# Performance work log

Measured on AMD Instinct MI355X. Metric: run time of the kernel, lower is better.

Reference implementation:

```python
import jax, jax.numpy as jnp
import numpy as np

D = 256      # n_feature
LVL = 17     # tree depth (leaf levels)
MIX = 20     # M mixture components


def _lstm_cell(x, h, c, Wih, Whh, bih, bhh):
    # torch.nn.LSTMCell gate order: i, f, g, o
    g = x @ Wih.T + bih + h @ Whh.T + bhh
    i, f, gg, o = jnp.split(g, 4, axis=1)
    c2 = jax.nn.sigmoid(f) * c + jax.nn.sigmoid(i) * jnp.tanh(gg)
    return jax.nn.sigmoid(o) * jnp.tanh(c2), c2


def _get_parameter(y, M):
    parts = jnp.split(y[:, :13 * M], 13, axis=1)
    pi = jax.nn.softmax(parts[0], axis=1)
    mu_x, mu_y = parts[1], parts[2]
    sx, sy = jnp.exp(parts[3]), jnp.exp(parts[4])
    rho_xy = jnp.tanh(parts[5])
    mu_a, mu_b = parts[6], parts[7]
    sa, sb = jnp.exp(parts[8]), jnp.exp(parts[9])
    rho_ab = jnp.tanh(parts[10])
    mu_s, ss = parts[11], jnp.exp(parts[12])
    q = jax.nn.softmax(y[:, -3:], axis=1)
    return (pi, mu_x, mu_y, sx, sy, rho_xy, mu_a, mu_b, sa, sb, rho_ab, mu_s, ss, q)


def _bvn_logpdf(dx, dy, mx, my, sx, sy, rho):
    zx = (dx - mx) / sx
    zy = (dy - my) / sy
    Z = zx ** 2 + zy ** 2 - 2.0 * rho * zx * zy
    return -Z / (2.0 * (1.0 - rho ** 2)) - jnp.log(2.0 * jnp.pi * sx * sy * jnp.sqrt(1.0 - rho ** 2))


def _nll(pt, prm):
    # pt: [n, 8] = (x, y, a, b, slope, p1, p2, p3); prm: GMM parameters, each [n, M]
    pi, mx, my, sx, sy, rxy, ma, mb, sa, sb, rab, ms, ss, q = prm
    lpi = jnp.log(pi)
    dx, dy, da, db, ds = (pt[:, k:k + 1] for k in range(5))
    p = pt[:, 5:8]
    lse = jax.scipy.special.logsumexp
    lxy = lse(lpi + _bvn_logpdf(dx, dy, mx, my, sx, sy, rxy), axis=1)
    lab = lse(lpi + _bvn_logpdf(da, db, ma, mb, sa, sb, rab), axis=1)
    lsl = lse(lpi - (ds - ms) ** 2 / (2.0 * ss ** 2) - jnp.log(jnp.sqrt(2.0 * jnp.pi) * ss), axis=1)
    pen = -(p * jnp.log(q)).sum(axis=1)
    return -(lxy + lab + lsl) + pen


def _expected_pos(prm):
    pi, mx, my, sx, sy, rxy, ma, mb, sa, sb, rab, ms, ss, q = prm
    e = lambda m: (pi * m).sum(axis=1)
    return jnp.concatenate([jnp.stack([e(mx), e(my), e(ma), e(mb), e(ms)], axis=1), q], axis=1)


def _levels(I_flat):
    # I_flat is bottom-up concatenation of per-level [ni,3] blocks of a full binary tree
    n_int = I_flat.shape[0]
    L = int(np.log2(n_int + 1))
    sizes = [2 ** (L - 1 - i) for i in range(L)]
    offs = np.concatenate([[0], np.cumsum(sizes)])
    return [I_flat[offs[i]:offs[i + 1]] for i in range(L)]


def setup_inputs() -> dict:
    key = jax.random.key(0)
    ks = jax.random.split(key, 16)
    N = 2 ** (LVL + 1) - 1  # 262143 total nodes
    # heap-layout full binary tree: children of i are 2i+1, 2i+2; bottom-up levels
    blocks = []
    for l in range(LVL - 1, -1, -1):
        f = np.arange(2 ** l - 1, 2 ** (l + 1) - 1)
        blocks.append(np.stack([2 * f + 1, 2 * f + 2, f], axis=1))
    I_flat = jnp.asarray(np.concatenate(blocks, 0), dtype=jnp.int32)
    s = 0.05
    return {
        "X": jax.random.normal(ks[0], (N, 8), jnp.float32),
        "Feature": jax.random.normal(ks[1], (N, D), jnp.float32),
        "I_flat": I_flat,
        "W_ih_e": jax.random.normal(ks[2], (4 * (D // 2), 8), jnp.float32) * s,
        "W_hh_e": jax.random.normal(ks[3], (4 * (D // 2), D // 2), jnp.float32) * s,
        "b_ih_e": jax.random.normal(ks[4], (4 * (D // 2),), jnp.float32) * s,
        "b_hh_e": jax.random.normal(ks[5], (4 * (D // 2),), jnp.float32) * s,
        "fc_h_W": jax.random.normal(ks[6], (2 * D, D), jnp.float32) * s,
        "fc_h_b": jax.random.normal(ks[7], (2 * D,), jnp.float32) * s,
        "W_ih_d": jax.random.normal(ks[8], (4 * D, D + 8), jnp.float32) * s,
        "W_hh_d": jax.random.normal(ks[9], (4 * D, D), jnp.float32) * s,
        "b_ih_d": jax.random.normal(ks[10], (4 * D,), jnp.float32) * s,
        "b_hh_d": jax.random.normal(ks[11], (4 * D,), jnp.float32) * s,
        "fc_W": jax.random.normal(ks[12], (13 * MIX + 3, D // 2), jnp.float32) * s,
        "fc_b": jax.random.normal(ks[13], (13 * MIX + 3,), jnp.float32) * s,
    }


def reference(X, Feature, I_flat, W_ih_e, W_hh_e, b_ih_e, b_hh_e,
              fc_h_W, fc_h_b, W_ih_d, W_hh_d, b_ih_d, b_hh_d, fc_W, fc_b):
    levels = _levels(I_flat)
    num_I = len(levels)

    # ---- encode: bottom-up gather children -> LSTMCell -> scatter father ----
    Feature_New = Feature
    for I in levels:
        li, ri, fi = I[:, 0], I[:, 1], I[:, 2]
        hl, cl = jnp.split(Feature[li], 2, axis=1)
        hr, cr = jnp.split(Feature[ri], 2, axis=1)
        hlo, clo = _lstm_cell(X[li], hl, cl, W_ih_e, W_hh_e, b_ih_e, b_hh_e)
        hro, cro = _lstm_cell(X[ri], hr, cr, W_ih_e, W_hh_e, b_ih_e, b_hh_e)
        out = jnp.concatenate([hlo + hro, clo + cro], axis=1)
        Feature_New = Feature_New.at[fi].set(out)

    # ---- decode: top-down gather father -> LSTMCell+GMM head -> scatter children ----
    X_P = X
    Feat = Feature_New
    Loss = jnp.float32(0.0)
    for I in reversed(levels):
        li, ri, fi = I[:, 0], I[:, 1], I[:, 2]
        p_l, p_r, p_f = X[li], X[ri], X[fi]
        f_f = Feat[fi]
        z = jnp.tanh(f_f @ fc_h_W.T + fc_h_b)
        h_f, c_f = jnp.split(z, 2, axis=1)
        h_o, c_o = _lstm_cell(jnp.concatenate([p_f, f_f], axis=1), h_f, c_f,
                              W_ih_d, W_hh_d, b_ih_d, b_hh_d)
        h_left, h_right = jnp.split(h_o, 2, axis=1)
        c_left, c_right = jnp.split(c_o, 2, axis=1)
        prm_l = _get_parameter(h_left @ fc_W.T + fc_b, MIX)
        prm_r = _get_parameter(h_right @ fc_W.T + fc_b, MIX)
        direct = _nll(p_l, prm_l) + _nll(p_r, prm_r)
        swapped = _nll(p_l, prm_r) + _nll(p_r, prm_l)
        sw = swapped < direct  # l_r_index == 1 -> swap left/right outputs
        Loss = Loss + jnp.mean(jnp.where(sw, swapped, direct))
        pos_l, pos_r = _expected_pos(prm_l), _expected_pos(prm_r)
        feat_l = jnp.concatenate([h_left, c_left], axis=1)
        feat_r = jnp.concatenate([h_right, c_right], axis=1)
        swc = sw[:, None]
        Feat = Feat.at[li].set(jnp.where(swc, feat_r, feat_l))
        Feat = Feat.at[ri].set(jnp.where(swc, feat_l, feat_r))
        X_P = X_P.at[li].set(jnp.where(swc, pos_r, pos_l))
        X_P = X_P.at[ri].set(jnp.where(swc, pos_l, pos_r))
    return Loss / num_I
```

## Files before the change

kernel.cpp:

```cpp
#include <hip/hip_runtime.h>
#include <hip/hip_bf16.h>
#include <math.h>


#define LOG2PI 1.8378770664093453f

typedef __attribute__((ext_vector_type(8))) short short8;
typedef __attribute__((ext_vector_type(4))) float f32x4;

__device__ inline float frcp(float x) { return __builtin_amdgcn_rcpf(x); }
__device__ inline float fexp(float x) { return __expf(x); }
__device__ inline float flog(float x) { return __logf(x); }
__device__ inline float ftanh(float x) {
    float xc = fminf(fmaxf(x, -10.f), 10.f);
    float e = __expf(2.f * xc);
    return (e - 1.f) * frcp(e + 1.f);
}
__device__ inline float sigm(float x) {
    float xc = fminf(fmaxf(x, -30.f), 30.f);
    return frcp(1.f + __expf(-xc));
}

__device__ inline ushort f2b(float v) {
    union { float f; unsigned u; } x; x.f = v;
    unsigned r = x.u + 0x7fffu + ((x.u >> 16) & 1u);
    return (ushort)(r >> 16);
}
__device__ inline float b2f(ushort h) {
    union { unsigned u; float f; } x; x.u = ((unsigned)h) << 16; return x.f;
}

__device__ inline void gload16(const void* g, void* l) {
    __builtin_amdgcn_global_load_lds(
        (const __attribute__((address_space(1))) unsigned*)g,
        (__attribute__((address_space(3))) unsigned*)l, 16, 0, 0);
}

__device__ inline f32x4 mfma16(short8 a, short8 b, f32x4 c) {
    return __builtin_amdgcn_mfma_f32_16x16x32_bf16(a, b, c, 0, 0, 0);
}

__device__ inline float halfmax(float v) {
    #pragma unroll
    for (int o = 16; o >= 1; o >>= 1) v = fmaxf(v, __shfl_xor(v, o));
    return v;
}
__device__ inline float halfsum(float v) {
    #pragma unroll
    for (int o = 16; o >= 1; o >>= 1) v += __shfl_xor(v, o);
    return v;
}
__device__ inline float lse20(float t) {
    float m = halfmax(t);
    float s = halfsum(fexp(t - m));
    return m + flog(s);
}

__device__ inline float nll_node(const float* yb, const float* X,
                                 long long fi, int lane, bool& sw_out)
{
    const int half = lane >> 5, k = lane & 31;
    float v = (k < 20) ? yb[k] : -INFINITY;
    float mm = halfmax(v);
    float se = halfsum((k < 20) ? fexp(v - mm) : 0.f);
    float lpi = v - mm - flog(se);
    float mx = 0, my = 0, rsx = 1, rsy = 1, rho = 0, hro = 0, cxy = 0;
    float ma = 0, mb2 = 0, rsa = 1, rsb = 1, rab = 0, hra = 0, cab = 0;
    float ms = 0, hrs = 0, csl = 0;
    if (k < 20) {
        mx = yb[20 + k]; my = yb[40 + k];
        float lsx = yb[60 + k], lsy = yb[80 + k];
        rsx = fexp(-lsx); rsy = fexp(-lsy);
        rho = ftanh(yb[100 + k]);
        float omr = 1.f - rho * rho;
        hro = 0.5f * frcp(omr);
        cxy = LOG2PI + lsx + lsy + 0.5f * flog(omr);
        ma = yb[120 + k]; mb2 = yb[140 + k];
        float lsa = yb[160 + k], lsb = yb[180 + k];
        rsa = fexp(-lsa); rsb = fexp(-lsb);
        rab = ftanh(yb[200 + k]);
        float omr2 = 1.f - rab * rab;
        hra = 0.5f * frcp(omr2);
        cab = LOG2PI + lsa + lsb + 0.5f * flog(omr2);
        ms = yb[220 + k]; float lss = yb[240 + k];
        float rss = fexp(-lss);
        hrs = 0.5f * rss * rss;
        csl = 0.5f * LOG2PI + lss;
    }
    float lq0, lq1, lq2;
    {
        float q0 = yb[260], q1 = yb[261], q2 = yb[262];
        float qm = fmaxf(q0, fmaxf(q1, q2));
        float l = flog(fexp(q0 - qm) + fexp(q1 - qm) + fexp(q2 - qm)) + qm;
        lq0 = q0 - l; lq1 = q1 - l; lq2 = q2 - l;
    }
    const float* pl = X + (size_t)(2 * fi + 1) * 8;
    const float* pr = X + (size_t)(2 * fi + 2) * 8;
    float res[2];
    #pragma unroll
    for (int s = 0; s < 2; ++s) {
        const float* pt = s ? pr : pl;
        float dx = pt[0], dy = pt[1], da = pt[2], db = pt[3], ds = pt[4];
        float t1 = -INFINITY, t2 = -INFINITY, t3 = -INFINITY;
        if (k < 20) {
            float zx = (dx - mx) * rsx, zy = (dy - my) * rsy;
            float Zz = zx * zx + zy * zy - 2.f * rho * zx * zy;
            t1 = lpi - Zz * hro - cxy;
            float za = (da - ma) * rsa, zb = (db - mb2) * rsb;
            float Z2 = za * za + zb * zb - 2.f * rab * za * zb;
            t2 = lpi - Z2 * hra - cab;
            float zs = ds - ms;
            t3 = lpi - zs * zs * hrs - csl;
        }
        float l1 = lse20(t1), l2 = lse20(t2), l3 = lse20(t3);
        float pen = -(pt[5] * lq0 + pt[6] * lq1 + pt[7] * lq2);
        res[s] = -(l1 + l2 + l3) + pen;
    }
    float Aval = half ? res[1] : res[0];
    float Bval = half ? res[0] : res[1];
    float direct = Aval + __shfl_xor(Aval, 32);
    float swapped = Bval + __shfl_xor(Bval, 32);
    sw_out = swapped < direct;
    return sw_out ? swapped : direct;
}

__device__ inline void feat_write_ap(ushort* Ap, const ushort* Hj,
                                     const ushort* Cj, long long fi, bool sw,
                                     int lane)
{
    const size_t rowL = 2 * (size_t)fi + 1;
    const int offL = sw ? 128 : 0;
    const int offR = 128 - offL;
    const int part = lane >> 5;
    const int c = (lane & 31) * 4;
    ushort4 vL = *(const ushort4*)((part ? Cj : Hj) + offL + c);
    ushort4 vR = *(const ushort4*)((part ? Cj : Hj) + offR + c);
    *(ushort4*)(Ap + rowL * 576 + 8 + part * 128 + c) = vL;
    *(ushort4*)(Ap + (rowL + 1) * 576 + 8 + part * 128 + c) = vR;
}

__global__ __launch_bounds__(256) void z_gemm(
    ushort* __restrict__ Apc,
    const ushort* __restrict__ Wz,
    const float* __restrict__ fc_h_b,
    ushort* __restrict__ Zcc,
    int M)
{
    __shared__ ushort As[128 * 64];
    __shared__ ushort Bs[128 * 64];
    const int tid = threadIdx.x;
    const int lane = tid & 63;
    const int w = tid >> 6;
    const int wr = w >> 1, wc = w & 1;
    const int fr = lane & 15, fq = lane >> 4;
    const int m0 = blockIdx.x * 128, n0 = blockIdx.y * 128;

    f32x4 acc[4][4] = {};

    #pragma unroll
    for (int k0 = 0; k0 < 256; k0 += 64) {
        __syncthreads();
        #pragma unroll
        for (int it = 0; it < 4; ++it) {
            const int i = it * 256 + tid;
            const int row = i >> 3, slot = i & 7;
            const int sl = slot ^ (row & 7);
            const int wbase = (i - lane) * 8;
            {
                int gm = m0 + row; gm = gm < M ? gm : M - 1;
                gload16(Apc + (size_t)gm * 576 + 8 + k0 + sl * 8, &As[wbase]);
            }
            {
                int gn = n0 + row; gn = gn < 512 ? gn : 511;
                gload16(Wz + (size_t)gn * 256 + k0 + sl * 8, &Bs[wbase]);
            }
        }
        __syncthreads();
        #pragma unroll
        for (int ks = 0; ks < 2; ++ks) {
            short8 af[4], bfr[4];
            #pragma unroll
            for (int mr = 0; mr < 4; ++mr) {
                const int row = wr * 64 + mr * 16 + fr;
                const int sl = (ks * 4 + fq) ^ (row & 7);
                af[mr] = *(const short8*)&As[row * 64 + sl * 8];
            }
            #pragma unroll
            for (int nc = 0; nc < 4; ++nc) {
                const int row = wc * 64 + nc * 16 + fr;
                const int sl = (ks * 4 + fq) ^ (row & 7);
                bfr[nc] = *(const short8*)&Bs[row * 64 + sl * 8];
            }
            #pragma unroll
            for (int mr = 0; mr < 4; ++mr)
                #pragma unroll
                for (int nc = 0; nc < 4; ++nc)
                    acc[mr][nc] = mfma16(af[mr], bfr[nc], acc[mr][nc]);
        }
    }

    #pragma unroll
    for (int mr = 0; mr < 4; ++mr) {
        #pragma unroll
        for (int j = 0; j < 4; ++j) {
            const int row = m0 + wr * 64 + mr * 16 + fq * 4 + j;
            if (row >= M) continue;
            #pragma unroll
            for (int nc = 0; nc < 4; ++nc) {
                const int col = n0 + wc * 64 + nc * 16 + fr;
                const float z = ftanh(acc[mr][nc][j] + fc_h_b[col]);
                if (col < 256)
                    Apc[(size_t)row * 576 + 264 + col] = f2b(z);
                else
                    Zcc[(size_t)row * 256 + (col - 256)] = f2b(z);
            }
        }
    }
}

__global__ __launch_bounds__(256) void gates_lstm(
    const ushort* __restrict__ Apc,
    const ushort* __restrict__ Wg,
    const float*  __restrict__ bg,
    const ushort* __restrict__ Zcc,
    ushort* __restrict__ H, ushort* __restrict__ C, int M)
{
    __shared__ ushort As[128 * 64];
    __shared__ ushort Bs[128 * 64];
    const int tid = threadIdx.x;
    const int lane = tid & 63;
    const int w = tid >> 6;
    const int wr = w >> 1, wc = w & 1;
    const int fr = lane & 15, fq = lane >> 4;
    const int m0 = blockIdx.x * 128, n0 = blockIdx.y * 128;

    f32x4 acc[4][4] = {};

    #pragma unroll
    for (int k0 = 0; k0 < 576; k0 += 64) {
        __syncthreads();
        #pragma unroll
        for (int it = 0; it < 4; ++it) {
            const int i = it * 256 + tid;
            const int row = i >> 3, slot = i & 7;
            const int sl = slot ^ (row & 7);
            const int wbase = (i - lane) * 8;
            {
                int gm = m0 + row; gm = gm < M ? gm : M - 1;
                gload16(Apc + (size_t)gm * 576 + k0 + sl * 8, &As[wbase]);
            }
            gload16(Wg + (size_t)(n0 + row) * 576 + k0 + sl * 8, &Bs[wbase]);
        }
        __syncthreads();
        #pragma unroll
        for (int ks = 0; ks < 2; ++ks) {
            short8 af[4], bfr[4];
            #pragma unroll
            for (int mr = 0; mr < 4; ++mr) {
                const int row = wr * 64 + mr * 16 + fr;
                const int sl = (ks * 4 + fq) ^ (row & 7);
                af[mr] = *(const short8*)&As[row * 64 + sl * 8];
            }
            #pragma unroll
            for (int nc = 0; nc < 4; ++nc) {
                const int row = wc * 64 + nc * 16 + fr;
                const int sl = (ks * 4 + fq) ^ (row & 7);
                bfr[nc] = *(const short8*)&Bs[row * 64 + sl * 8];
            }
            #pragma unroll
            for (int mr = 0; mr < 4; ++mr)
                #pragma unroll
                for (int nc = 0; nc < 4; ++nc)
                    acc[mr][nc] = mfma16(af[mr], bfr[nc], acc[mr][nc]);
        }
    }

    const int q = fr & 3;
    #pragma unroll
    for (int mr = 0; mr < 4; ++mr) {
        const int node = m0 + wr * 64 + mr * 16 + fq * 4 + q;
        #pragma unroll
        for (int nc = 0; nc < 4; ++nc) {
            const int col = n0 + wc * 64 + nc * 16 + fr;
            f32x4 v = acc[mr][nc];
            const float b = bg[col];
            v[0] += b; v[1] += b; v[2] += b; v[3] += b;
            float gv[4];
            gv[q] = v[q];
            #pragma unroll
            for (int m = 1; m < 4; ++m)
                gv[q ^ m] = __shfl_xor(v[q ^ m], m);
            if (node < M) {
                const int t = (col >> 2) & 255;
                const float cf = b2f(Zcc[(size_t)node * 256 + t]);
                const float c2 = sigm(gv[1]) * cf + sigm(gv[0]) * ftanh(gv[2]);
                const float hv = sigm(gv[3]) * ftanh(c2);
                H[(size_t)node * 256 + t] = f2b(hv);
                C[(size_t)node * 256 + t] = f2b(c2);
            }
        }
    }
}

__global__ __launch_bounds__(256) void ynll(
    const ushort* __restrict__ Hb, const ushort* __restrict__ Cc,
    const ushort* __restrict__ Wyp,
    const float* __restrict__ fc_b, const float* __restrict__ X,
    ushort* __restrict__ Ap, float* __restrict__ loss,
    int Bc, long long nb_fi, float scale, int writeFeat)
{
    __shared__ ushort Hs[32 * 128];
    __shared__ float Ys[32][324];
    __shared__ float lsum[4];
    const int tid = threadIdx.x;
    const int lane = tid & 63;
    const int wv = tid >> 6;
    const int fr = lane & 15, fq = lane >> 4;
    const int n16 = blockIdx.x * 16;

    #pragma unroll
    for (int it = 0; it < 2; ++it) {
        const int i = it * 256 + tid;
        const int row = i >> 4, slot = i & 15;
        const int sl = slot ^ (row & 7);
        int gr = n16 * 2 + row;
        const int grmax = 2 * Bc - 1;
        gr = gr <= grmax ? gr : grmax;
        gload16(Hb + (size_t)gr * 128 + sl * 8, &Hs[(i - lane) * 8]);
    }
    __syncthreads();

    f32x4 acc[2][5] = {};
    #pragma unroll
    for (int ks = 0; ks < 4; ++ks) {
        short8 a[2];
        #pragma unroll
        for (int rf = 0; rf < 2; ++rf) {
            const int row = rf * 16 + fr;
            const int sl = (ks * 4 + fq) ^ (row & 7);
            a[rf] = *(const short8*)&Hs[row * 128 + sl * 8];
        }
        #pragma unroll
        for (int n = 0; n < 5; ++n) {
            const short8 b = *(const short8*)(
                Wyp + (size_t)(wv * 80 + n * 16 + fr) * 128 + ks * 32 + fq * 8);
            acc[0][n] = mfma16(a[0], b, acc[0][n]);
            acc[1][n] = mfma16(a[1], b, acc[1][n]);
        }
    }
    #pragma unroll
    for (int rf = 0; rf < 2; ++rf)
        #pragma unroll
        for (int n = 0; n < 5; ++n)
            #pragma unroll
            for (int j = 0; j < 4; ++j) {
                const int row = rf * 16 + fq * 4 + j;
                const int col = wv * 80 + n * 16 + fr;
                Ys[row][col] = acc[rf][n][j] + (col < 263 ? fc_b[col] : 0.f);
            }
    __syncthreads();

    float wsum = 0.f;
    #pragma unroll
    for (int s4 = 0; s4 < 4; ++s4) {
        const int jj = wv * 4 + s4;
        const int j = n16 + jj;
        if (j >= Bc) break;
        bool sw;
        const long long fi = nb_fi + j;
        wsum += nll_node(Ys[2 * jj + (lane >> 5)], X, fi, lane, sw);
        if (writeFeat)
            feat_write_ap(Ap, Hb + (size_t)j * 256, Cc + (size_t)j * 256,
                          fi, sw, lane);
    }
    if (lane == 0) lsum[wv] = wsum;
    __syncthreads();
    if (tid == 0)
        atomicAdd(loss, (lsum[0] + lsum[1] + lsum[2] + lsum[3]) * scale);
}

__global__ __launch_bounds__(256) void pack_all(
    const float* __restrict__ fc_h_W, ushort* __restrict__ Wz,
    const float* __restrict__ Wih, const float* __restrict__ Whh,
    ushort* __restrict__ Wg,
    const float* __restrict__ bih, const float* __restrict__ bhh,
    float* __restrict__ bg,
    const float* __restrict__ fcW, ushort* __restrict__ Wy,
    const float* __restrict__ X, ushort* __restrict__ Ap, int nInt)
{
    int i = blockIdx.x * 256 + threadIdx.x;
    if (i < 131072) { Wz[i] = f2b(fc_h_W[i]); return; }
    i -= 131072;
    if (i < 589824) {
        int np = i / 576, c = i - np * 576;
        int n = (np & 3) * 256 + (np >> 2);
        float v = 0.f;
        if (c < 264) v = Wih[n * 264 + c];
        else if (c < 520) v = Whh[n * 256 + (c - 264)];
        Wg[i] = f2b(v);
        return;
    }
    i -= 589824;
    if (i < 1024) {
        int n = (i & 3) * 256 + (i >> 2);
        bg[i] = bih[n] + bhh[n];
        return;
    }
    i -= 1024;
    if (i < 40960) {
        int r = i / 128;
        Wy[i] = f2b(r < 263 ? fcW[i] : 0.f);
        return;
    }
    i -= 40960;
    if (i < nInt * 64) {
        int row = i >> 6, c = i & 63;
        if (c < 8) Ap[(size_t)row * 576 + c] = f2b(X[row * 8 + c]);
        else       Ap[(size_t)row * 576 + 512 + c] = 0;
    }
}

__global__ __launch_bounds__(256) void encoder_root(
    const float* __restrict__ X, const float* __restrict__ Feature,
    const float* __restrict__ Wih, const float* __restrict__ Whh,
    const float* __restrict__ bih, const float* __restrict__ bhh,
    ushort* __restrict__ Ap)
{
    __shared__ float gsh[2][512];
    __shared__ float hc[2][256];
    const int t = threadIdx.x;
    for (int ch = 0; ch < 2; ++ch) {
        const int node = 1 + ch;
        const float* x = X + node * 8;
        const float* h = Feature + (size_t)node * 256;
        #pragma unroll
        for (int gi = 0; gi < 2; ++gi) {
            int g = t + gi * 256;
            float s = bih[g] + bhh[g];
            const float* wi = Wih + (size_t)g * 8;
            #pragma unroll
            for (int k = 0; k < 8; ++k) s += wi[k] * x[k];
            const float* wh = Whh + (size_t)g * 128;
            for (int k = 0; k < 128; ++k) s += wh[k] * h[k];
            gsh[ch][g] = s;
        }
    }
    __syncthreads();
    {
        int ch = t >> 7, u = t & 127;
        float i_ = gsh[ch][u], f_ = gsh[ch][128 + u];
        float gg = gsh[ch][256 + u], o_ = gsh[ch][384 + u];
        float c = Feature[(size_t)(1 + ch) * 256 + 128 + u];
        float c2 = sigm(f_) * c + sigm(i_) * ftanh(gg);
        hc[ch][u] = sigm(o_) * ftanh(c2);
        hc[ch][128 + u] = c2;
    }
    __syncthreads();
    Ap[8 + t] = f2b(hc[0][t] + hc[1][t]);
}

extern "C" void kernel_launch(void* const* d_in, const int* in_sizes, int n_in,
                              void* d_out, int out_size, void* d_ws, size_t ws_size,
                              hipStream_t stream)
{
    const float* X       = (const float*)d_in[0];
    const float* Feature = (const float*)d_in[1];
    const float* W_ih_e  = (const float*)d_in[3];
    const float* W_hh_e  = (const float*)d_in[4];
    const float* b_ih_e  = (const float*)d_in[5];
    const float* b_hh_e  = (const float*)d_in[6];
    const float* fc_h_W  = (const float*)d_in[7];
    const float* fc_h_b  = (const float*)d_in[8];
    const float* W_ih_d  = (const float*)d_in[9];
    const float* W_hh_d  = (const float*)d_in[10];
    const float* b_ih_d  = (const float*)d_in[11];
    const float* b_hh_d  = (const float*)d_in[12];
    const float* fc_W    = (const float*)d_in[13];
    const float* fc_b    = (const float*)d_in[14];
    const int Nnodes = in_sizes[0] / 8;
    const int nInt = (Nnodes - 1) / 2;

    float* out = (float*)d_out;
    hipMemsetAsync(d_out, 0, sizeof(float), stream);

    char* cur = (char*)d_ws;
    auto take = [&](size_t bytes) {
        char* p = cur;
        cur += (bytes + 255) & ~(size_t)255;
        return p;
    };
    ushort* Ap = (ushort*)take((size_t)(nInt + 1) * 576 * 2);
    ushort* Wz = (ushort*)take((size_t)512 * 256 * 2);
    ushort* Wg = (ushort*)take((size_t)1024 * 576 * 2);
    ushort* Wy = (ushort*)take((size_t)320 * 128 * 2);
    float*  bg = (float*) take((size_t)1024 * 4);
    const size_t fixed_used = (size_t)(cur - (char*)d_ws);
    int CB = 65536;
    while (CB > 8192 && fixed_used + (size_t)CB * 1536 + 4096 > ws_size) CB >>= 1;
    ushort* Zcc = (ushort*)take((size_t)CB * 256 * 2);
    ushort* Hb  = (ushort*)take((size_t)CB * 256 * 2);
    ushort* Cc  = (ushort*)take((size_t)CB * 256 * 2);

    const int packTotal = 131072 + 589824 + 1024 + 40960 + nInt * 64;
    pack_all<<<(packTotal + 255) / 256, 256, 0, stream>>>(
        fc_h_W, Wz, W_ih_d, W_hh_d, Wg, b_ih_d, b_hh_d, bg, fc_W, Wy,
        X, Ap, nInt);

    encoder_root<<<1, 256, 0, stream>>>(X, Feature, W_ih_e, W_hh_e,
                                        b_ih_e, b_hh_e, Ap);

    for (int l = 0; l < 17; ++l) {
        const int B = 1 << l;
        const long long nb = B - 1;
        const int writeFeat = (l < 16) ? 1 : 0;
        const float scale = 1.f / ((float)B * 17.f);
        for (int j0 = 0; j0 < B; j0 += CB) {
            const int Bc = (B - j0 < CB) ? (B - j0) : CB;
            const int mg = (Bc + 127) / 128;
            ushort* Apc = Ap + (size_t)(nb + j0) * 576;
            z_gemm<<<dim3(mg, 4), 256, 0, stream>>>(Apc, Wz, fc_h_b, Zcc, Bc);
            gates_lstm<<<dim3(mg, 8), 256, 0, stream>>>(
                Apc, Wg, bg, Zcc, Hb, Cc, Bc);
            ynll<<<(Bc + 15) / 16, 256, 0, stream>>>(
                Hb, Cc, Wy, fc_b, X, Ap, out,
                Bc, nb + j0, scale, writeFeat);
        }
    }
}
```

Before: 1.316 ms.

## Fuse next-level z_gemm into ynll epilogue and drop chunked launches

The per-level z_gemm launch is removed. Each ynll block now computes the tanh(fc_h) projection for the child rows it just wrote, storing them into Ap and Zcc for the next level, with a single z_gemm launched for the root. The Y logits are kept in shared memory as bf16, so one aliased pool can hold H, Y and the feature tiles. Chunking by CB is dropped and Zcc/Hb/Cc are sized to a fixed 65536 rows, which assumes the workspace is large enough. The Ap padding init is also vectorised. This cuts one launch per level and an extra global round trip, but it adds serial GEMM work to the tail of ynll and lowers Y precision.

```diff
diff --git a/kernel.cpp b/kernel.cpp
--- a/kernel.cpp
+++ b/kernel.cpp
@@ -56,11 +56,11 @@
     return m + flog(s);
 }
 
-__device__ inline float nll_node(const float* yb, const float* X,
+__device__ inline float nll_node(const ushort* yb, const float* X,
                                  long long fi, int lane, bool& sw_out)
 {
     const int half = lane >> 5, k = lane & 31;
-    float v = (k < 20) ? yb[k] : -INFINITY;
+    float v = (k < 20) ? b2f(yb[k]) : -INFINITY;
     float mm = halfmax(v);
     float se = halfsum((k < 20) ? fexp(v - mm) : 0.f);
     float lpi = v - mm - flog(se);
@@ -68,28 +68,28 @@
     float ma = 0, mb2 = 0, rsa = 1, rsb = 1, rab = 0, hra = 0, cab = 0;
     float ms = 0, hrs = 0, csl = 0;
     if (k < 20) {
-        mx = yb[20 + k]; my = yb[40 + k];
-        float lsx = yb[60 + k], lsy = yb[80 + k];
+        mx = b2f(yb[20 + k]); my = b2f(yb[40 + k]);
+        float lsx = b2f(yb[60 + k]), lsy = b2f(yb[80 + k]);
         rsx = fexp(-lsx); rsy = fexp(-lsy);
-        rho = ftanh(yb[100 + k]);
+        rho = ftanh(b2f(yb[100 + k]));
         float omr = 1.f - rho * rho;
         hro = 0.5f * frcp(omr);
         cxy = LOG2PI + lsx + lsy + 0.5f * flog(omr);
-        ma = yb[120 + k]; mb2 = yb[140 + k];
-        float lsa = yb[160 + k], lsb = yb[180 + k];
+        ma = b2f(yb[120 + k]); mb2 = b2f(yb[140 + k]);
+        float lsa = b2f(yb[160 + k]), lsb = b2f(yb[180 + k]);
         rsa = fexp(-lsa); rsb = fexp(-lsb);
-        rab = ftanh(yb[200 + k]);
+        rab = ftanh(b2f(yb[200 + k]));
         float omr2 = 1.f - rab * rab;
         hra = 0.5f * frcp(omr2);
         cab = LOG2PI + lsa + lsb + 0.5f * flog(omr2);
-        ms = yb[220 + k]; float lss = yb[240 + k];
+        ms = b2f(yb[220 + k]); float lss = b2f(yb[240 + k]);
         float rss = fexp(-lss);
         hrs = 0.5f * rss * rss;
         csl = 0.5f * LOG2PI + lss;
     }
     float lq0, lq1, lq2;
     {
-        float q0 = yb[260], q1 = yb[261], q2 = yb[262];
+        float q0 = b2f(yb[260]), q1 = b2f(yb[261]), q2 = b2f(yb[262]);
         float qm = fmaxf(q0, fmaxf(q1, q2));
         float l = flog(fexp(q0 - qm) + fexp(q1 - qm) + fexp(q2 - qm)) + qm;
         lq0 = q0 - l; lq1 = q1 - l; lq2 = q2 - l;
@@ -302,16 +302,22 @@
     }
 }
 
-__global__ __launch_bounds__(256) void ynll(
+#define YS 272
+__global__ __launch_bounds__(256) void ynll_z(
     const ushort* __restrict__ Hb, const ushort* __restrict__ Cc,
     const ushort* __restrict__ Wyp,
     const float* __restrict__ fc_b, const float* __restrict__ X,
-    ushort* __restrict__ Ap, float* __restrict__ loss,
+    ushort* __restrict__ Ap,
+    const ushort* __restrict__ Wz, const float* __restrict__ fc_h_b,
+    ushort* __restrict__ Zcc,
+    float* __restrict__ loss,
     int Bc, long long nb_fi, float scale, int writeFeat)
 {
-    __shared__ ushort Hs[32 * 128];
-    __shared__ float Ys[32][324];
+    __shared__ char pool[17408] __attribute__((aligned(16)));
     __shared__ float lsum[4];
+    ushort* Hs  = (ushort*)pool;
+    ushort* Ysb = (ushort*)pool;
+    ushort* Fs  = (ushort*)pool;
     const int tid = threadIdx.x;
     const int lane = tid & 63;
     const int wv = tid >> 6;
@@ -348,6 +354,8 @@
             acc[1][n] = mfma16(a[1], b, acc[1][n]);
         }
     }
+    __syncthreads();
+
     #pragma unroll
     for (int rf = 0; rf < 2; ++rf)
         #pragma unroll
@@ -356,7 +364,8 @@
             for (int j = 0; j < 4; ++j) {
                 const int row = rf * 16 + fq * 4 + j;
                 const int col = wv * 80 + n * 16 + fr;
-                Ys[row][col] = acc[rf][n][j] + (col < 263 ? fc_b[col] : 0.f);
+                if (col < 263)
+                    Ysb[row * YS + col] = f2b(acc[rf][n][j] + fc_b[col]);
             }
     __syncthreads();
 
@@ -368,7 +377,7 @@
         if (j >= Bc) break;
         bool sw;
         const long long fi = nb_fi + j;
-        wsum += nll_node(Ys[2 * jj + (lane >> 5)], X, fi, lane, sw);
+        wsum += nll_node(&Ysb[(2 * jj + (lane >> 5)) * YS], X, fi, lane, sw);
         if (writeFeat)
             feat_write_ap(Ap, Hb + (size_t)j * 256, Cc + (size_t)j * 256,
                           fi, sw, lane);
@@ -377,6 +386,53 @@
     __syncthreads();
     if (tid == 0)
         atomicAdd(loss, (lsum[0] + lsum[1] + lsum[2] + lsum[3]) * scale);
+
+    if (!writeFeat) return;
+
+    const size_t base = 2 * (size_t)(nb_fi + n16) + 1;
+    const int rmax = 2 * Bc - 2 * n16 - 1;
+    #pragma unroll
+    for (int it = 0; it < 4; ++it) {
+        const int i = it * 256 + tid;
+        const int row = i >> 5, slot = i & 31;
+        const int sl = slot ^ (row & 7);
+        int r = row; r = r <= rmax ? r : rmax;
+        gload16(Ap + (base + r) * 576 + 8 + sl * 8, &Fs[(i - lane) * 8]);
+    }
+    __syncthreads();
+
+    f32x4 zacc[2][8] = {};
+    for (int ks = 0; ks < 8; ++ks) {
+        short8 a[2];
+        #pragma unroll
+        for (int mf = 0; mf < 2; ++mf) {
+            const int r = mf * 16 + fr;
+            const int ss = (ks * 4 + fq) ^ (r & 7);
+            a[mf] = *(const short8*)&Fs[r * 256 + ss * 8];
+        }
+        #pragma unroll
+        for (int nf = 0; nf < 8; ++nf) {
+            const short8 b = *(const short8*)(
+                Wz + (size_t)(wv * 128 + nf * 16 + fr) * 256 + ks * 32 + fq * 8);
+            zacc[0][nf] = mfma16(a[0], b, zacc[0][nf]);
+            zacc[1][nf] = mfma16(a[1], b, zacc[1][nf]);
+        }
+    }
+    #pragma unroll
+    for (int mf = 0; mf < 2; ++mf)
+        #pragma unroll
+        for (int nf = 0; nf < 8; ++nf)
+            #pragma unroll
+            for (int j = 0; j < 4; ++j) {
+                const int r = mf * 16 + fq * 4 + j;
+                if (r > rmax) continue;
+                const int col = wv * 128 + nf * 16 + fr;
+                const float z = ftanh(zacc[mf][nf][j] + fc_h_b[col]);
+                if (col < 256)
+                    Ap[(base + r) * 576 + 264 + col] = f2b(z);
+                else
+                    Zcc[(size_t)(2 * n16 + r) * 256 + (col - 256)] = f2b(z);
+            }
 }
 
 __global__ __launch_bounds__(256) void pack_all(
@@ -413,10 +469,19 @@
         return;
     }
     i -= 40960;
-    if (i < nInt * 64) {
-        int row = i >> 6, c = i & 63;
-        if (c < 8) Ap[(size_t)row * 576 + c] = f2b(X[row * 8 + c]);
-        else       Ap[(size_t)row * 576 + 512 + c] = 0;
+    if (i < nInt * 8) {
+        int row = i >> 3, s = i & 7;
+        if (s == 0) {
+            const float* xs = X + (size_t)row * 8;
+            short8 v;
+            #pragma unroll
+            for (int k = 0; k < 8; ++k)
+                ((ushort*)&v)[k] = f2b(xs[k]);
+            *(short8*)(Ap + (size_t)row * 576) = v;
+        } else {
+            short8 z = {0, 0, 0, 0, 0, 0, 0, 0};
+            *(short8*)(Ap + (size_t)row * 576 + (64 + s) * 8) = z;
+        }
     }
 }
 
@@ -489,41 +554,35 @@
         cur += (bytes + 255) & ~(size_t)255;
         return p;
     };
-    ushort* Ap = (ushort*)take((size_t)(nInt + 1) * 576 * 2);
-    ushort* Wz = (ushort*)take((size_t)512 * 256 * 2);
-    ushort* Wg = (ushort*)take((size_t)1024 * 576 * 2);
-    ushort* Wy = (ushort*)take((size_t)320 * 128 * 2);
-    float*  bg = (float*) take((size_t)1024 * 4);
-    const size_t fixed_used = (size_t)(cur - (char*)d_ws);
-    int CB = 65536;
-    while (CB > 8192 && fixed_used + (size_t)CB * 1536 + 4096 > ws_size) CB >>= 1;
-    ushort* Zcc = (ushort*)take((size_t)CB * 256 * 2);
-    ushort* Hb  = (ushort*)take((size_t)CB * 256 * 2);
-    ushort* Cc  = (ushort*)take((size_t)CB * 256 * 2);
-
-    const int packTotal = 131072 + 589824 + 1024 + 40960 + nInt * 64;
+    ushort* Ap  = (ushort*)take((size_t)(nInt + 1) * 576 * 2);
+    ushort* Wz  = (ushort*)take((size_t)512 * 256 * 2);
+    ushort* Wg  = (ushort*)take((size_t)1024 * 576 * 2);
+    ushort* Wy  = (ushort*)take((size_t)320 * 128 * 2);
+    float*  bg  = (float*) take((size_t)1024 * 4);
+    ushort* Zcc = (ushort*)take((size_t)65536 * 256 * 2);
+    ushort* Hb  = (ushort*)take((size_t)65536 * 256 * 2);
+    ushort* Cc  = (ushort*)take((size_t)65536 * 256 * 2);
+
+    const int packTotal = 131072 + 589824 + 1024 + 40960 + nInt * 8;
     pack_all<<<(packTotal + 255) / 256, 256, 0, stream>>>(
         fc_h_W, Wz, W_ih_d, W_hh_d, Wg, b_ih_d, b_hh_d, bg, fc_W, Wy,
         X, Ap, nInt);
 
     encoder_root<<<1, 256, 0, stream>>>(X, Feature, W_ih_e, W_hh_e,
                                         b_ih_e, b_hh_e, Ap);
+
+    z_gemm<<<dim3(1, 4), 256, 0, stream>>>(Ap, Wz, fc_h_b, Zcc, 1);
 
     for (int l = 0; l < 17; ++l) {
         const int B = 1 << l;
         const long long nb = B - 1;
         const int writeFeat = (l < 16) ? 1 : 0;
         const float scale = 1.f / ((float)B * 17.f);
-        for (int j0 = 0; j0 < B; j0 += CB) {
-            const int Bc = (B - j0 < CB) ? (B - j0) : CB;
-            const int mg = (Bc + 127) / 128;
-            ushort* Apc = Ap + (size_t)(nb + j0) * 576;
-            z_gemm<<<dim3(mg, 4), 256, 0, stream>>>(Apc, Wz, fc_h_b, Zcc, Bc);
-            gates_lstm<<<dim3(mg, 8), 256, 0, stream>>>(
-                Apc, Wg, bg, Zcc, Hb, Cc, Bc);
-            ynll<<<(Bc + 15) / 16, 256, 0, stream>>>(
-                Hb, Cc, Wy, fc_b, X, Ap, out,
-                Bc, nb + j0, scale, writeFeat);
-        }
-    }
-}
+        const int mg = (B + 127) / 128;
+        gates_lstm<<<dim3(mg, 8), 256, 0, stream>>>(
+            Ap + (size_t)nb * 576, Wg, bg, Zcc, Hb, Cc, B);
+        ynll_z<<<(B + 15) / 16, 256, 0, stream>>>(
+            Hb, Cc, Wy, fc_b, X, Ap, Wz, fc_h_b, Zcc, out,
+            B, nb, scale, writeFeat);
+    }
+}
```

New measurement: 1.383 ms. +5.1%, slower.
